# Kernel optimization log

Measured on AMD Instinct MI355X. Metric: run time of the kernel, lower is better.

Reference implementation:

```python
import jax, jax.numpy as jnp
import numpy as np

B, T, S, H, M, V, L = 16, 128, 256, 512, 512, 32000, 2


def setup_inputs() -> dict:
    key = jax.random.key(0)
    ks = jax.random.split(key, 16)
    s = 0.05
    embed = jax.random.normal(ks[3], (V, H), jnp.float32) * 0.02
    embed = embed.at[0].set(0.0)  # padding_idx=0 row is zero in nn.Embedding
    return {
        'tgt': jax.random.randint(ks[0], (B, T), 0, V),
        'hidden': jax.random.normal(ks[1], (L, B, M), jnp.float32) * 0.1,
        'enc_outs': jax.random.normal(ks[2], (B, S, M), jnp.float32) * 0.1,
        'embed': embed,
        'W_ih0': jax.random.normal(ks[4], (3 * M, H), jnp.float32) * s,
        'W_hh0': jax.random.normal(ks[5], (3 * M, M), jnp.float32) * s,
        'b_ih0': jax.random.normal(ks[6], (3 * M,), jnp.float32) * s,
        'b_hh0': jax.random.normal(ks[7], (3 * M,), jnp.float32) * s,
        'W_ih1': jax.random.normal(ks[8], (3 * M, M), jnp.float32) * s,
        'W_hh1': jax.random.normal(ks[9], (3 * M, M), jnp.float32) * s,
        'b_ih1': jax.random.normal(ks[10], (3 * M,), jnp.float32) * s,
        'b_hh1': jax.random.normal(ks[11], (3 * M,), jnp.float32) * s,
        'W_out': jax.random.normal(ks[12], (V, M), jnp.float32) * s,
        'b_out': jax.random.normal(ks[13], (V,), jnp.float32) * s,
    }


def _gru_layer(x, h0, W_ih, W_hh, b_ih, b_hh):
    """PyTorch-convention GRU layer. x: [B,T,in], h0: [B,M] -> (ys [B,T,M], hT [B,M])."""
    # precompute input-side gates for all timesteps: [B,T,3M]
    xg = jnp.einsum('bti,gi->btg', x, W_ih) + b_ih

    def step(h, xg_t):
        gh = h @ W_hh.T + b_hh
        i_r, i_z, i_n = jnp.split(xg_t, 3, axis=-1)
        h_r, h_z, h_n = jnp.split(gh, 3, axis=-1)
        r = jax.nn.sigmoid(i_r + h_r)
        z = jax.nn.sigmoid(i_z + h_z)
        n = jnp.tanh(i_n + r * h_n)
        h_new = (1.0 - z) * n + z * h
        return h_new, h_new

    hT, ys = jax.lax.scan(step, h0, jnp.swapaxes(xg, 0, 1))  # scan over time
    return jnp.swapaxes(ys, 0, 1), hT


def reference(tgt, hidden, enc_outs, embed, W_ih0, W_hh0, b_ih0, b_hh0,
              W_ih1, W_hh1, b_ih1, b_hh1, W_out, b_out):
    x = embed[tgt]  # [B,T,H]
    out0, h0f = _gru_layer(x, hidden[0], W_ih0, W_hh0, b_ih0, b_hh0)
    outputs, h1f = _gru_layer(out0, hidden[1], W_ih1, W_hh1, b_ih1, b_hh1)  # [B,T,M]
    hn = jnp.stack([h0f, h1f])  # [L,B,M]
    cn = jnp.zeros_like(hn)
    # dot-product attention, batched over all timesteps (fuses the per-ts Python loop)
    scores = jnp.einsum('btm,bsm->bts', outputs, enc_outs)
    weights = jax.nn.softmax(scores, axis=-1)
    contexts = jnp.einsum('bts,bsm->btm', weights, enc_outs)
    attn_outs = outputs + contexts
    logits = jnp.einsum('btm,vm->btv', attn_outs, W_out) + b_out  # dropout p=0 -> identity
    return logits, (hn, cn)
```

## Files before the change

kernel.cpp:

```cpp
#include <hip/hip_runtime.h>
#include <hip/hip_bf16.h>
#include <math.h>

#define B_ 16
#define T_ 128
#define S_ 256
#define H_ 512
#define M_ 512
#define V_ 32000

typedef __attribute__((ext_vector_type(8))) short short8v;
typedef __attribute__((ext_vector_type(4))) float float4v;

__global__ __launch_bounds__(128) void k_gather(const int* __restrict__ tgt,
    const float* __restrict__ embed, float* __restrict__ x)
{
  const int row = blockIdx.x;
  const int v = tgt[row];
  const float4* src = (const float4*)(embed + (size_t)v * H_);
  float4* dst = (float4*)(x + (size_t)row * H_);
  dst[threadIdx.x] = src[threadIdx.x];
}

__global__ __launch_bounds__(256) void k_gemm_nt_bias(const float* __restrict__ A,
    const float* __restrict__ Bm, const float* __restrict__ bias,
    float* __restrict__ C, int N)
{
  __shared__ float As[64][33];
  __shared__ float Bs[64][33];
  const int tid = threadIdx.x;
  const int tm = tid >> 4, tn = tid & 15;
  const float* Ab = A  + (size_t)blockIdx.y * 64 * 512;
  const float* Bb = Bm + (size_t)blockIdx.x * 64 * 512;
  float acc00=0.f,acc01=0.f,acc02=0.f,acc03=0.f;
  float acc10=0.f,acc11=0.f,acc12=0.f,acc13=0.f;
  float acc20=0.f,acc21=0.f,acc22=0.f,acc23=0.f;
  float acc30=0.f,acc31=0.f,acc32=0.f,acc33=0.f;
  for (int k0 = 0; k0 < 512; k0 += 32) {
#pragma unroll
    for (int i = 0; i < 8; ++i) {
      int v = tid + i * 256;
      int row = v >> 5, col = v & 31;
      As[row][col] = Ab[(size_t)row * 512 + k0 + col];
      Bs[row][col] = Bb[(size_t)row * 512 + k0 + col];
    }
    __syncthreads();
#pragma unroll
    for (int kk = 0; kk < 32; ++kk) {
      float a0 = As[tm*4+0][kk], a1 = As[tm*4+1][kk];
      float a2 = As[tm*4+2][kk], a3 = As[tm*4+3][kk];
      float b0 = Bs[tn*4+0][kk], b1 = Bs[tn*4+1][kk];
      float b2 = Bs[tn*4+2][kk], b3 = Bs[tn*4+3][kk];
      acc00 += a0*b0; acc01 += a0*b1; acc02 += a0*b2; acc03 += a0*b3;
      acc10 += a1*b0; acc11 += a1*b1; acc12 += a1*b2; acc13 += a1*b3;
      acc20 += a2*b0; acc21 += a2*b1; acc22 += a2*b2; acc23 += a2*b3;
      acc30 += a3*b0; acc31 += a3*b1; acc32 += a3*b2; acc33 += a3*b3;
    }
    __syncthreads();
  }
  const int mbase = blockIdx.y*64 + tm*4;
  const int nbase = blockIdx.x*64 + tn*4;
  float bj0 = bias[nbase+0], bj1 = bias[nbase+1], bj2 = bias[nbase+2], bj3 = bias[nbase+3];
  float* Cr0 = C + (size_t)(mbase+0)*N + nbase;
  float* Cr1 = C + (size_t)(mbase+1)*N + nbase;
  float* Cr2 = C + (size_t)(mbase+2)*N + nbase;
  float* Cr3 = C + (size_t)(mbase+3)*N + nbase;
  Cr0[0]=acc00+bj0; Cr0[1]=acc01+bj1; Cr0[2]=acc02+bj2; Cr0[3]=acc03+bj3;
  Cr1[0]=acc10+bj0; Cr1[1]=acc11+bj1; Cr1[2]=acc12+bj2; Cr1[3]=acc13+bj3;
  Cr2[0]=acc20+bj0; Cr2[1]=acc21+bj1; Cr2[2]=acc22+bj2; Cr2[3]=acc23+bj3;
  Cr3[0]=acc30+bj0; Cr3[1]=acc31+bj1; Cr3[2]=acc32+bj2; Cr3[3]=acc33+bj3;
}

__device__ inline void bulk8_to_lds(const float* rowbase, int sc, float* dstrow)
{
  const float* p = rowbase + sc * 4;
  float4 a, b, c, d, e, f, g, h;
  asm volatile(
    "global_load_dwordx4 %0, %[p], off sc0 sc1\n\t"
    "global_load_dwordx4 %1, %[p], off offset:256 sc0 sc1\n\t"
    "global_load_dwordx4 %2, %[p], off offset:512 sc0 sc1\n\t"
    "global_load_dwordx4 %3, %[p], off offset:768 sc0 sc1\n\t"
    "global_load_dwordx4 %4, %[p], off offset:1024 sc0 sc1\n\t"
    "global_load_dwordx4 %5, %[p], off offset:1280 sc0 sc1\n\t"
    "global_load_dwordx4 %6, %[p], off offset:1536 sc0 sc1\n\t"
    "global_load_dwordx4 %7, %[p], off offset:1792 sc0 sc1\n\t"
    "s_waitcnt vmcnt(0)"
    : "=&v"(a), "=&v"(b), "=&v"(c), "=&v"(d),
      "=&v"(e), "=&v"(f), "=&v"(g), "=&v"(h)
    : [p]"v"(p)
    : "memory");
  *(float4*)&dstrow[(0*16 + sc) * 4] = a;
  *(float4*)&dstrow[(1*16 + sc) * 4] = b;
  *(float4*)&dstrow[(2*16 + sc) * 4] = c;
  *(float4*)&dstrow[(3*16 + sc) * 4] = d;
  *(float4*)&dstrow[(4*16 + sc) * 4] = e;
  *(float4*)&dstrow[(5*16 + sc) * 4] = f;
  *(float4*)&dstrow[(6*16 + sc) * 4] = g;
  *(float4*)&dstrow[(7*16 + sc) * 4] = h;
}

__global__ __launch_bounds__(256) void k_gru2(
    const float* __restrict__ xg0,
    const float* __restrict__ Whh0, const float* __restrict__ bhh0,
    const float* __restrict__ Wih1, const float* __restrict__ bih1,
    const float* __restrict__ Whh1, const float* __restrict__ bhh1,
    const float* __restrict__ hidden,
    float* __restrict__ out0, float* __restrict__ y1, float* __restrict__ hn,
    unsigned int* __restrict__ fA, unsigned int* __restrict__ fB)
{
  __shared__ float Wl[24][520];
  __shared__ float hx[2][16 * 520];
  __shared__ float ps[24][16][17];
  const int bid = blockIdx.x;
  const int lt = threadIdx.x;

  if (bid >= 192) {
    __shared__ int done;
    if (lt == 0) done = 0;
    __syncthreads();
    const unsigned int* flag = &fB[(T_ - 1) * 128 + (bid - 192)];
    float a0 = 1.0f + lt, a1 = 2.0f + lt, a2 = 3.0f, a3 = 4.0f;
    const float mb = 1.0001f, cb = 0.9999f;
    for (;;) {
#pragma unroll 16
      for (int i = 0; i < 512; ++i) {
        a0 = __builtin_fmaf(a0, mb, cb); a1 = __builtin_fmaf(a1, mb, cb);
        a2 = __builtin_fmaf(a2, mb, cb); a3 = __builtin_fmaf(a3, mb, cb);
      }
      if (lt == 0 &&
          __hip_atomic_load(flag, __ATOMIC_RELAXED, __HIP_MEMORY_SCOPE_AGENT) != 0u)
        done = 1;
      __syncthreads();
      if (done) break;
    }
    asm volatile("" :: "v"(a0), "v"(a1), "v"(a2), "v"(a3));
    return;
  }

  const bool isB = bid >= 64;
  const int wg = isB ? bid - 64 : bid;
  const int dbase = isB ? wg * 4 : wg * 8;

  for (int r = 0; r < 24; ++r) {
    const float* src;
    if (!isB) src = Whh0 + (size_t)((r >> 3) * 512 + dbase + (r & 7)) * 512;
    else if (r < 12) src = Whh1 + (size_t)((r >> 2) * 512 + dbase + (r & 3)) * 512;
    else { int rr = r - 12; src = Wih1 + (size_t)((rr >> 2) * 512 + dbase + (rr & 3)) * 512; }
    Wl[r][lt] = src[lt];
    Wl[r][lt + 256] = src[lt + 256];
  }

  const int kq = lt & 15;
  const int bq = (lt >> 4) & 3;
  const int rgrp = lt >> 6;
  const int sb = lt >> 4;
  const int sc = lt & 15;
  float* ybuf = isB ? y1 : out0;
  const float* h0g = hidden + (isB ? 8192 : 0);

  const int rb = isB ? (lt >> 2) : (lt >> 3);
  const int rdl = isB ? (lt & 3) : (lt & 7);
  const int rdg = dbase + rdl;
  const int nred = isB ? 64 : 128;
  float bhr = 0.f, bhz = 0.f, bhn = 0.f, bir = 0.f, biz = 0.f, bin_ = 0.f;
  if (lt < nred) {
    const float* bhh = isB ? bhh1 : bhh0;
    bhr = bhh[rdg]; bhz = bhh[512 + rdg]; bhn = bhh[1024 + rdg];
    if (isB) { bir = bih1[rdg]; biz = bih1[512 + rdg]; bin_ = bih1[1024 + rdg]; }
  }

  for (int t = 0; t < T_; ++t) {
    if (!isB) {
      if (t > 0 && lt < 64) {
        unsigned v;
        do {
          v = __hip_atomic_load(&fA[(t - 1) * 64 + lt], __ATOMIC_RELAXED, __HIP_MEMORY_SCOPE_AGENT);
          if (__all(v != 0u)) break;
          __builtin_amdgcn_s_sleep(1);
        } while (true);
      }
    } else {
      if (lt < 64) {
        unsigned v;
        do {
          v = __hip_atomic_load(&fA[t * 64 + lt], __ATOMIC_RELAXED, __HIP_MEMORY_SCOPE_AGENT);
          if (__all(v != 0u)) break;
          __builtin_amdgcn_s_sleep(1);
        } while (true);
      } else if (t > 0 && lt < 192) {
        unsigned v;
        do {
          v = __hip_atomic_load(&fB[(t - 1) * 128 + (lt - 64)], __ATOMIC_RELAXED, __HIP_MEMORY_SCOPE_AGENT);
          if (__all(v != 0u)) break;
          __builtin_amdgcn_s_sleep(1);
        } while (true);
      }
    }
    __syncthreads();

    if (t == 0) {
#pragma unroll
      for (int j = 0; j < 8; ++j)
        *(float4*)&hx[0][sb * 520 + (j * 16 + sc) * 4] =
            *(const float4*)(h0g + sb * 512 + (j * 16 + sc) * 4);
    } else {
      bulk8_to_lds(ybuf + (size_t)(sb * T_ + t - 1) * 512, sc, &hx[0][sb * 520]);
    }
    if (isB)
      bulk8_to_lds(out0 + (size_t)(sb * T_ + t) * 512, sc, &hx[1][sb * 520]);
    __syncthreads();

    const float* inb = (isB && rgrp >= 2) ? &hx[1][0] : &hx[0][0];
    float acc[6][4];
#pragma unroll
    for (int jr = 0; jr < 6; ++jr)
#pragma unroll
      for (int jb = 0; jb < 4; ++jb) acc[jr][jb] = 0.f;
#pragma unroll
    for (int i = 0; i < 8; ++i) {
      const int kb = kq * 4 + i * 64;
      float4 hv0 = *(const float4*)(inb + (bq * 4 + 0) * 520 + kb);
      float4 hv1 = *(const float4*)(inb + (bq * 4 + 1) * 520 + kb);
      float4 hv2 = *(const float4*)(inb + (bq * 4 + 2) * 520 + kb);
      float4 hv3 = *(const float4*)(inb + (bq * 4 + 3) * 520 + kb);
#pragma unroll
      for (int jr = 0; jr < 6; ++jr) {
        float4 wv = *(const float4*)(&Wl[rgrp * 6 + jr][kb]);
        acc[jr][0] += wv.x*hv0.x + wv.y*hv0.y + wv.z*hv0.z + wv.w*hv0.w;
        acc[jr][1] += wv.x*hv1.x + wv.y*hv1.y + wv.z*hv1.z + wv.w*hv1.w;
        acc[jr][2] += wv.x*hv2.x + wv.y*hv2.y + wv.z*hv2.z + wv.w*hv2.w;
        acc[jr][3] += wv.x*hv3.x + wv.y*hv3.y + wv.z*hv3.z + wv.w*hv3.w;
      }
    }
#pragma unroll
    for (int jr = 0; jr < 6; ++jr)
#pragma unroll
      for (int jb = 0; jb < 4; ++jb)
        ps[rgrp * 6 + jr][bq * 4 + jb][kq] = acc[jr][jb];
    __syncthreads();

    if (lt < nred) {
      float ghr, ghz, ghn, ixr, ixz, ixn;
      if (!isB) {
        float s0 = 0.f, s1 = 0.f, s2 = 0.f;
#pragma unroll
        for (int q = 0; q < 16; ++q) {
          s0 += ps[rdl][rb][q];
          s1 += ps[8 + rdl][rb][q];
          s2 += ps[16 + rdl][rb][q];
        }
        ghr = s0 + bhr; ghz = s1 + bhz; ghn = s2 + bhn;
        const float* xrow = xg0 + (size_t)(rb * T_ + t) * 1536;
        ixr = xrow[rdg]; ixz = xrow[512 + rdg]; ixn = xrow[1024 + rdg];
      } else {
        float s0=0.f,s1=0.f,s2=0.f,s3=0.f,s4=0.f,s5=0.f;
#pragma unroll
        for (int q = 0; q < 16; ++q) {
          s0 += ps[rdl][rb][q];       s1 += ps[4 + rdl][rb][q];  s2 += ps[8 + rdl][rb][q];
          s3 += ps[12 + rdl][rb][q];  s4 += ps[16 + rdl][rb][q]; s5 += ps[20 + rdl][rb][q];
        }
        ghr = s0 + bhr; ghz = s1 + bhz; ghn = s2 + bhn;
        ixr = s3 + bir; ixz = s4 + biz; ixn = s5 + bin_;
      }
      float rr = 1.f / (1.f + expf(-(ixr + ghr)));
      float zz = 1.f / (1.f + expf(-(ixz + ghz)));
      float nn = tanhf(ixn + rr * ghn);
      float hp = hx[0][rb * 520 + rdg];
      float hnew = (1.f - zz) * nn + zz * hp;
      __hip_atomic_store(&ybuf[(size_t)(rb * T_ + t) * 512 + rdg], hnew,
                         __ATOMIC_RELAXED, __HIP_MEMORY_SCOPE_AGENT);
      if (t == T_ - 1) hn[(isB ? 8192 : 0) + rb * 512 + rdg] = hnew;
    }
    __syncthreads();
    if (lt == 0) {
      if (isB)
        __hip_atomic_store(&fB[t * 128 + wg], 1u, __ATOMIC_RELAXED, __HIP_MEMORY_SCOPE_AGENT);
      else
        __hip_atomic_store(&fA[t * 64 + wg], 1u, __ATOMIC_RELAXED, __HIP_MEMORY_SCOPE_AGENT);
    }
  }
}

__global__ __launch_bounds__(256) void k_attn(const float* __restrict__ y,
    const float* __restrict__ enc, float* __restrict__ aout)
{
  __shared__ float orow[512];
  __shared__ float wbuf[256];
  __shared__ float red[8];
  const int row = blockIdx.x;
  const int b = row >> 7;
  const int lt = threadIdx.x;
  orow[lt]       = y[(size_t)row*512 + lt];
  orow[lt + 256] = y[(size_t)row*512 + lt + 256];
  __syncthreads();
  const float* er = enc + (size_t)(b*S_ + lt) * 512;
  float acc = 0.f;
  for (int k = 0; k < 512; k += 4) {
    float4 e = *(const float4*)(er + k);
    acc += orow[k]*e.x + orow[k+1]*e.y + orow[k+2]*e.z + orow[k+3]*e.w;
  }
  float m = acc;
#pragma unroll
  for (int off = 32; off > 0; off >>= 1) m = fmaxf(m, __shfl_down(m, off));
  if ((lt & 63) == 0) red[lt >> 6] = m;
  __syncthreads();
  float mx = fmaxf(fmaxf(red[0], red[1]), fmaxf(red[2], red[3]));
  float e = expf(acc - mx);
  wbuf[lt] = e;
  float s = e;
#pragma unroll
  for (int off = 32; off > 0; off >>= 1) s += __shfl_down(s, off);
  if ((lt & 63) == 0) red[4 + (lt >> 6)] = s;
  __syncthreads();
  const float inv = 1.f / (red[4] + red[5] + red[6] + red[7]);
  const int kk = lt * 2;
  float c0 = 0.f, c1 = 0.f;
  for (int s2 = 0; s2 < S_; ++s2) {
    float ws = wbuf[s2];
    float2 ev = *(const float2*)(enc + (size_t)(b*S_ + s2)*512 + kk);
    c0 += ws * ev.x; c1 += ws * ev.y;
  }
  aout[(size_t)row*512 + kk]     = orow[kk]     + c0 * inv;
  aout[(size_t)row*512 + kk + 1] = orow[kk + 1] + c1 * inv;
}

__global__ __launch_bounds__(256) void k_logits(const float* __restrict__ A,
    const float* __restrict__ Bm, const float* __restrict__ bias,
    float* __restrict__ C)
{
  __shared__ unsigned short Bs[128 * 512];
  __shared__ unsigned short As[128 * 64];
  const int tid = threadIdx.x;
  const int nbase = blockIdx.x * 128;
  const int wv = tid >> 6;
  const int l  = tid & 63;
  const int wr = wv >> 1, wc = wv & 1;
  const int r = l & 15, q = l >> 4;

  for (int i = 0; i < 32; ++i) {
    const int gid = tid + i * 256;
    const int row = gid >> 6, cg = gid & 63;
    const float* Bg = Bm + (size_t)(nbase + row) * 512 + cg * 8;
    float4 g0 = *(const float4*)(Bg);
    float4 g1 = *(const float4*)(Bg + 4);
    union { short8v v; __hip_bfloat162 h2[4]; } pb;
    pb.h2[0] = __float22bfloat162_rn({g0.x, g0.y});
    pb.h2[1] = __float22bfloat162_rn({g0.z, g0.w});
    pb.h2[2] = __float22bfloat162_rn({g1.x, g1.y});
    pb.h2[3] = __float22bfloat162_rn({g1.z, g1.w});
    const int byte = (row * 1024 + cg * 16) ^ ((row & 7) << 4);
    *(short8v*)&Bs[byte >> 1] = pb.v;
  }
  __syncthreads();

  for (int m = 0; m < 16; ++m) {
    const int mbase = m * 128;
    float4v acc[4][4];
#pragma unroll
    for (int mi = 0; mi < 4; ++mi)
#pragma unroll
      for (int ni = 0; ni < 4; ++ni)
        acc[mi][ni] = (float4v){0.f, 0.f, 0.f, 0.f};

    for (int kc = 0; kc < 8; ++kc) {
#pragma unroll
      for (int i = 0; i < 4; ++i) {
        const int gid = tid + i * 256;
        const int row = gid >> 3, cg = gid & 7;
        const float* Ag = A + (size_t)(mbase + row) * 512 + kc * 64 + cg * 8;
        float4 f0 = *(const float4*)(Ag);
        float4 f1 = *(const float4*)(Ag + 4);
        union { short8v v; __hip_bfloat162 h2[4]; } pa;
        pa.h2[0] = __float22bfloat162_rn({f0.x, f0.y});
        pa.h2[1] = __float22bfloat162_rn({f0.z, f0.w});
        pa.h2[2] = __float22bfloat162_rn({f1.x, f1.y});
        pa.h2[3] = __float22bfloat162_rn({f1.z, f1.w});
        const int byte = (row * 128 + cg * 16) ^ ((row & 7) << 4);
        *(short8v*)&As[byte >> 1] = pa.v;
      }
      __syncthreads();

#pragma unroll
      for (int k0s = 0; k0s < 2; ++k0s) {
        short8v af[4], bf[4];
#pragma unroll
        for (int mi = 0; mi < 4; ++mi) {
          const int row = wr * 64 + mi * 16 + r;
          const int byte = (row * 128 + k0s * 64 + q * 16) ^ ((row & 7) << 4);
          af[mi] = *(short8v*)&As[byte >> 1];
        }
#pragma unroll
        for (int ni = 0; ni < 4; ++ni) {
          const int row = wc * 64 + ni * 16 + r;
          const int byte = (row * 1024 + kc * 128 + k0s * 64 + q * 16) ^ ((row & 7) << 4);
          bf[ni] = *(short8v*)&Bs[byte >> 1];
        }
#pragma unroll
        for (int mi = 0; mi < 4; ++mi)
#pragma unroll
          for (int ni = 0; ni < 4; ++ni)
            acc[mi][ni] = __builtin_amdgcn_mfma_f32_16x16x32_bf16(af[mi], bf[ni], acc[mi][ni], 0, 0, 0);
      }
      __syncthreads();
    }

    const int mg = mbase + wr * 64;
    const int ng = nbase + wc * 64;
#pragma unroll
    for (int ni = 0; ni < 4; ++ni) {
      const int col = ng + ni * 16 + r;
      const float bj = bias[col];
#pragma unroll
      for (int mi = 0; mi < 4; ++mi) {
        const int rowb = mg + mi * 16 + q * 4;
        float4v v = acc[mi][ni];
        C[(size_t)(rowb + 0) * V_ + col] = v[0] + bj;
        C[(size_t)(rowb + 1) * V_ + col] = v[1] + bj;
        C[(size_t)(rowb + 2) * V_ + col] = v[2] + bj;
        C[(size_t)(rowb + 3) * V_ + col] = v[3] + bj;
      }
    }
  }
}

extern "C" void kernel_launch(void* const* d_in, const int* in_sizes, int n_in,
                              void* d_out, int out_size, void* d_ws, size_t ws_size,
                              hipStream_t stream)
{
  const int*   tgt    = (const int*)  d_in[0];
  const float* hidden = (const float*)d_in[1];
  const float* enc    = (const float*)d_in[2];
  const float* embed  = (const float*)d_in[3];
  const float* W_ih0  = (const float*)d_in[4];
  const float* W_hh0  = (const float*)d_in[5];
  const float* b_ih0  = (const float*)d_in[6];
  const float* b_hh0  = (const float*)d_in[7];
  const float* W_ih1  = (const float*)d_in[8];
  const float* W_hh1  = (const float*)d_in[9];
  const float* b_ih1  = (const float*)d_in[10];
  const float* b_hh1  = (const float*)d_in[11];
  const float* W_out  = (const float*)d_in[12];
  const float* b_out  = (const float*)d_in[13];
  float* out = (float*)d_out;

  float* ws   = (float*)d_ws;
  float* xbuf = ws;
  float* xg   = ws + 1048576;
  float* out0 = xg + 3145728;
  float* y1   = out0 + 1048576;
  unsigned int* fA = (unsigned int*)(y1 + 1048576);
  unsigned int* fB = fA + T_ * 64;

  const size_t logitsN = (size_t)(B_*T_) * V_;
  float* hn = out + logitsN;
  float* cn = hn + 16384;

  hipMemsetAsync(fA, 0, (size_t)(T_ * 64 + T_ * 128) * sizeof(unsigned int), stream);
  hipMemsetAsync(cn, 0, (size_t)16384 * sizeof(float), stream);

  k_gather<<<dim3(B_*T_), dim3(128), 0, stream>>>(tgt, embed, xbuf);
  k_gemm_nt_bias<<<dim3(1536/64, (B_*T_)/64), dim3(256), 0, stream>>>(xbuf, W_ih0, b_ih0, xg, 1536);
  k_gru2<<<dim3(256), dim3(256), 0, stream>>>(xg, W_hh0, b_hh0, W_ih1, b_ih1,
                                              W_hh1, b_hh1, hidden, out0, y1, hn, fA, fB);
  k_attn<<<dim3(B_*T_), dim3(256), 0, stream>>>(y1, enc, xbuf);
  k_logits<<<dim3(V_/128), dim3(256), 0, stream>>>(xbuf, W_out, b_out, out);
}
```

Before: 1.403 ms.

## Replace GRU flag barriers with sentinel-filled data polling; fuse gather into bf16 MFMA GEMM

The per-step flag arrays and their spin waits are replaced by pre-filling out0/y1 with a NaN sentinel, so consumers poll the data itself until no sentinel remains. This removes one round of flag store/load latency per timestep in the serial recurrence. Separately, the embedding gather is fused into the input-projection GEMM, which now converts to bf16 and uses MFMA instead of scalar fp32. The cost is an extra fill kernel and reduced precision for the input gates, and correctness relies on the sentinel never occurring as a real value and on the 128-byte loads not tearing.

```diff
diff --git a/kernel.cpp b/kernel.cpp
--- a/kernel.cpp
+++ b/kernel.cpp
@@ -8,73 +8,108 @@
 #define H_ 512
 #define M_ 512
 #define V_ 32000
+#define SENT 0x7FC0DEADu
 
 typedef __attribute__((ext_vector_type(8))) short short8v;
 typedef __attribute__((ext_vector_type(4))) float float4v;
 
-__global__ __launch_bounds__(128) void k_gather(const int* __restrict__ tgt,
-    const float* __restrict__ embed, float* __restrict__ x)
-{
-  const int row = blockIdx.x;
-  const int v = tgt[row];
-  const float4* src = (const float4*)(embed + (size_t)v * H_);
-  float4* dst = (float4*)(x + (size_t)row * H_);
-  dst[threadIdx.x] = src[threadIdx.x];
-}
-
-__global__ __launch_bounds__(256) void k_gemm_nt_bias(const float* __restrict__ A,
-    const float* __restrict__ Bm, const float* __restrict__ bias,
-    float* __restrict__ C, int N)
-{
-  __shared__ float As[64][33];
-  __shared__ float Bs[64][33];
+__global__ __launch_bounds__(512) void k_fill(unsigned int* __restrict__ p, int n)
+{
+  const int i = blockIdx.x * 512 + threadIdx.x;
+  if (i < n) p[i] = SENT;
+}
+
+__global__ __launch_bounds__(256) void k_xg_bf16(const int* __restrict__ tgt,
+    const float* __restrict__ embed, const float* __restrict__ Bm,
+    const float* __restrict__ bias, float* __restrict__ C)
+{
+  __shared__ unsigned short As[128 * 40];
+  __shared__ unsigned short Bs[128 * 40];
   const int tid = threadIdx.x;
-  const int tm = tid >> 4, tn = tid & 15;
-  const float* Ab = A  + (size_t)blockIdx.y * 64 * 512;
-  const float* Bb = Bm + (size_t)blockIdx.x * 64 * 512;
-  float acc00=0.f,acc01=0.f,acc02=0.f,acc03=0.f;
-  float acc10=0.f,acc11=0.f,acc12=0.f,acc13=0.f;
-  float acc20=0.f,acc21=0.f,acc22=0.f,acc23=0.f;
-  float acc30=0.f,acc31=0.f,acc32=0.f,acc33=0.f;
+  const int nbase = blockIdx.x * 128;
+  const int mbase = blockIdx.y * 128;
+  const int wv = tid >> 6;
+  const int l  = tid & 63;
+  const int wr = wv >> 1, wc = wv & 1;
+  const int r = l & 15, q = l >> 4;
+
+  const int row0 = tid >> 2, row1 = (tid + 256) >> 2;
+  const int v0 = tgt[mbase + row0];
+  const int v1 = tgt[mbase + row1];
+
+  float4v acc[4][4];
+#pragma unroll
+  for (int mi = 0; mi < 4; ++mi)
+#pragma unroll
+    for (int ni = 0; ni < 4; ++ni)
+      acc[mi][ni] = (float4v){0.f, 0.f, 0.f, 0.f};
+
   for (int k0 = 0; k0 < 512; k0 += 32) {
-#pragma unroll
-    for (int i = 0; i < 8; ++i) {
-      int v = tid + i * 256;
-      int row = v >> 5, col = v & 31;
-      As[row][col] = Ab[(size_t)row * 512 + k0 + col];
-      Bs[row][col] = Bb[(size_t)row * 512 + k0 + col];
-    }
-    __syncthreads();
-#pragma unroll
-    for (int kk = 0; kk < 32; ++kk) {
-      float a0 = As[tm*4+0][kk], a1 = As[tm*4+1][kk];
-      float a2 = As[tm*4+2][kk], a3 = As[tm*4+3][kk];
-      float b0 = Bs[tn*4+0][kk], b1 = Bs[tn*4+1][kk];
-      float b2 = Bs[tn*4+2][kk], b3 = Bs[tn*4+3][kk];
-      acc00 += a0*b0; acc01 += a0*b1; acc02 += a0*b2; acc03 += a0*b3;
-      acc10 += a1*b0; acc11 += a1*b1; acc12 += a1*b2; acc13 += a1*b3;
-      acc20 += a2*b0; acc21 += a2*b1; acc22 += a2*b2; acc23 += a2*b3;
-      acc30 += a3*b0; acc31 += a3*b1; acc32 += a3*b2; acc33 += a3*b3;
-    }
-    __syncthreads();
-  }
-  const int mbase = blockIdx.y*64 + tm*4;
-  const int nbase = blockIdx.x*64 + tn*4;
-  float bj0 = bias[nbase+0], bj1 = bias[nbase+1], bj2 = bias[nbase+2], bj3 = bias[nbase+3];
-  float* Cr0 = C + (size_t)(mbase+0)*N + nbase;
-  float* Cr1 = C + (size_t)(mbase+1)*N + nbase;
-  float* Cr2 = C + (size_t)(mbase+2)*N + nbase;
-  float* Cr3 = C + (size_t)(mbase+3)*N + nbase;
-  Cr0[0]=acc00+bj0; Cr0[1]=acc01+bj1; Cr0[2]=acc02+bj2; Cr0[3]=acc03+bj3;
-  Cr1[0]=acc10+bj0; Cr1[1]=acc11+bj1; Cr1[2]=acc12+bj2; Cr1[3]=acc13+bj3;
-  Cr2[0]=acc20+bj0; Cr2[1]=acc21+bj1; Cr2[2]=acc22+bj2; Cr2[3]=acc23+bj3;
-  Cr3[0]=acc30+bj0; Cr3[1]=acc31+bj1; Cr3[2]=acc32+bj2; Cr3[3]=acc33+bj3;
-}
-
-__device__ inline void bulk8_to_lds(const float* rowbase, int sc, float* dstrow)
-{
+    __syncthreads();
+#pragma unroll
+    for (int h = 0; h < 2; ++h) {
+      const int c = tid + h * 256;
+      const int row = h ? row1 : row0;
+      const int av  = h ? v1 : v0;
+      const int cb = c & 3;
+      const float* Ag = embed + (size_t)av * 512 + k0 + cb * 8;
+      float4 f0 = *(const float4*)(Ag);
+      float4 f1 = *(const float4*)(Ag + 4);
+      union { short8v v; __hip_bfloat162 h2[4]; } pa;
+      pa.h2[0] = __float22bfloat162_rn({f0.x, f0.y});
+      pa.h2[1] = __float22bfloat162_rn({f0.z, f0.w});
+      pa.h2[2] = __float22bfloat162_rn({f1.x, f1.y});
+      pa.h2[3] = __float22bfloat162_rn({f1.z, f1.w});
+      *(short8v*)&As[row * 40 + cb * 8] = pa.v;
+      const float* Bg = Bm + (size_t)(nbase + row) * 512 + k0 + cb * 8;
+      float4 g0 = *(const float4*)(Bg);
+      float4 g1 = *(const float4*)(Bg + 4);
+      union { short8v v; __hip_bfloat162 h2[4]; } pb;
+      pb.h2[0] = __float22bfloat162_rn({g0.x, g0.y});
+      pb.h2[1] = __float22bfloat162_rn({g0.z, g0.w});
+      pb.h2[2] = __float22bfloat162_rn({g1.x, g1.y});
+      pb.h2[3] = __float22bfloat162_rn({g1.z, g1.w});
+      *(short8v*)&Bs[row * 40 + cb * 8] = pb.v;
+    }
+    __syncthreads();
+
+    short8v af[4], bf[4];
+#pragma unroll
+    for (int mi = 0; mi < 4; ++mi)
+      af[mi] = *(short8v*)&As[(wr * 64 + mi * 16 + r) * 40 + q * 8];
+#pragma unroll
+    for (int ni = 0; ni < 4; ++ni)
+      bf[ni] = *(short8v*)&Bs[(wc * 64 + ni * 16 + r) * 40 + q * 8];
+#pragma unroll
+    for (int mi = 0; mi < 4; ++mi)
+#pragma unroll
+      for (int ni = 0; ni < 4; ++ni)
+        acc[mi][ni] = __builtin_amdgcn_mfma_f32_16x16x32_bf16(af[mi], bf[ni], acc[mi][ni], 0, 0, 0);
+  }
+
+  const int mg = mbase + wr * 64;
+  const int ng = nbase + wc * 64;
+#pragma unroll
+  for (int ni = 0; ni < 4; ++ni) {
+    const int col = ng + ni * 16 + r;
+    const float bj = bias[col];
+#pragma unroll
+    for (int mi = 0; mi < 4; ++mi) {
+      const int rowb = mg + mi * 16 + q * 4;
+      float4v v = acc[mi][ni];
+      C[(size_t)(rowb + 0) * 1536 + col] = v[0] + bj;
+      C[(size_t)(rowb + 1) * 1536 + col] = v[1] + bj;
+      C[(size_t)(rowb + 2) * 1536 + col] = v[2] + bj;
+      C[(size_t)(rowb + 3) * 1536 + col] = v[3] + bj;
+    }
+  }
+}
+
+struct F4x8 { float4 a, b, c, d, e, f, g, h; };
+__device__ inline F4x8 bulk8_ld(const float* rowbase, int sc)
+{
+  F4x8 r;
   const float* p = rowbase + sc * 4;
-  float4 a, b, c, d, e, f, g, h;
   asm volatile(
     "global_load_dwordx4 %0, %[p], off sc0 sc1\n\t"
     "global_load_dwordx4 %1, %[p], off offset:256 sc0 sc1\n\t"
@@ -85,18 +120,38 @@
     "global_load_dwordx4 %6, %[p], off offset:1536 sc0 sc1\n\t"
     "global_load_dwordx4 %7, %[p], off offset:1792 sc0 sc1\n\t"
     "s_waitcnt vmcnt(0)"
-    : "=&v"(a), "=&v"(b), "=&v"(c), "=&v"(d),
-      "=&v"(e), "=&v"(f), "=&v"(g), "=&v"(h)
+    : "=&v"(r.a), "=&v"(r.b), "=&v"(r.c), "=&v"(r.d),
+      "=&v"(r.e), "=&v"(r.f), "=&v"(r.g), "=&v"(r.h)
     : [p]"v"(p)
     : "memory");
-  *(float4*)&dstrow[(0*16 + sc) * 4] = a;
-  *(float4*)&dstrow[(1*16 + sc) * 4] = b;
-  *(float4*)&dstrow[(2*16 + sc) * 4] = c;
-  *(float4*)&dstrow[(3*16 + sc) * 4] = d;
-  *(float4*)&dstrow[(4*16 + sc) * 4] = e;
-  *(float4*)&dstrow[(5*16 + sc) * 4] = f;
-  *(float4*)&dstrow[(6*16 + sc) * 4] = g;
-  *(float4*)&dstrow[(7*16 + sc) * 4] = h;
+  return r;
+}
+
+__device__ inline bool anysent(const F4x8& r)
+{
+  auto c1 = [](float4 v) {
+    return (__float_as_uint(v.x) == SENT) | (__float_as_uint(v.y) == SENT) |
+           (__float_as_uint(v.z) == SENT) | (__float_as_uint(v.w) == SENT);
+  };
+  return c1(r.a) | c1(r.b) | c1(r.c) | c1(r.d) |
+         c1(r.e) | c1(r.f) | c1(r.g) | c1(r.h);
+}
+
+__device__ inline void stage_sent(const float* rowbase, int sc, float* dstrow)
+{
+  F4x8 r = bulk8_ld(rowbase, sc);
+  while (anysent(r)) {
+    __builtin_amdgcn_s_sleep(1);
+    r = bulk8_ld(rowbase, sc);
+  }
+  *(float4*)&dstrow[(0*16 + sc) * 4] = r.a;
+  *(float4*)&dstrow[(1*16 + sc) * 4] = r.b;
+  *(float4*)&dstrow[(2*16 + sc) * 4] = r.c;
+  *(float4*)&dstrow[(3*16 + sc) * 4] = r.d;
+  *(float4*)&dstrow[(4*16 + sc) * 4] = r.e;
+  *(float4*)&dstrow[(5*16 + sc) * 4] = r.f;
+  *(float4*)&dstrow[(6*16 + sc) * 4] = r.g;
+  *(float4*)&dstrow[(7*16 + sc) * 4] = r.h;
 }
 
 __global__ __launch_bounds__(256) void k_gru2(
@@ -105,8 +160,7 @@
     const float* __restrict__ Wih1, const float* __restrict__ bih1,
     const float* __restrict__ Whh1, const float* __restrict__ bhh1,
     const float* __restrict__ hidden,
-    float* __restrict__ out0, float* __restrict__ y1, float* __restrict__ hn,
-    unsigned int* __restrict__ fA, unsigned int* __restrict__ fB)
+    float* __restrict__ out0, float* __restrict__ y1, float* __restrict__ hn)
 {
   __shared__ float Wl[24][520];
   __shared__ float hx[2][16 * 520];
@@ -118,7 +172,7 @@
     __shared__ int done;
     if (lt == 0) done = 0;
     __syncthreads();
-    const unsigned int* flag = &fB[(T_ - 1) * 128 + (bid - 192)];
+    const float* flag = y1 + (size_t)(15 * T_ + 127) * 512 + 511;
     float a0 = 1.0f + lt, a1 = 2.0f + lt, a2 = 3.0f, a3 = 4.0f;
     const float mb = 1.0001f, cb = 0.9999f;
     for (;;) {
@@ -128,7 +182,8 @@
         a2 = __builtin_fmaf(a2, mb, cb); a3 = __builtin_fmaf(a3, mb, cb);
       }
       if (lt == 0 &&
-          __hip_atomic_load(flag, __ATOMIC_RELAXED, __HIP_MEMORY_SCOPE_AGENT) != 0u)
+          __float_as_uint(__hip_atomic_load(flag, __ATOMIC_RELAXED,
+                                            __HIP_MEMORY_SCOPE_AGENT)) != SENT)
         done = 1;
       __syncthreads();
       if (done) break;
@@ -168,46 +223,19 @@
     bhr = bhh[rdg]; bhz = bhh[512 + rdg]; bhn = bhh[1024 + rdg];
     if (isB) { bir = bih1[rdg]; biz = bih1[512 + rdg]; bin_ = bih1[1024 + rdg]; }
   }
+  __syncthreads();
 
   for (int t = 0; t < T_; ++t) {
-    if (!isB) {
-      if (t > 0 && lt < 64) {
-        unsigned v;
-        do {
-          v = __hip_atomic_load(&fA[(t - 1) * 64 + lt], __ATOMIC_RELAXED, __HIP_MEMORY_SCOPE_AGENT);
-          if (__all(v != 0u)) break;
-          __builtin_amdgcn_s_sleep(1);
-        } while (true);
-      }
-    } else {
-      if (lt < 64) {
-        unsigned v;
-        do {
-          v = __hip_atomic_load(&fA[t * 64 + lt], __ATOMIC_RELAXED, __HIP_MEMORY_SCOPE_AGENT);
-          if (__all(v != 0u)) break;
-          __builtin_amdgcn_s_sleep(1);
-        } while (true);
-      } else if (t > 0 && lt < 192) {
-        unsigned v;
-        do {
-          v = __hip_atomic_load(&fB[(t - 1) * 128 + (lt - 64)], __ATOMIC_RELAXED, __HIP_MEMORY_SCOPE_AGENT);
-          if (__all(v != 0u)) break;
-          __builtin_amdgcn_s_sleep(1);
-        } while (true);
-      }
-    }
-    __syncthreads();
-
     if (t == 0) {
 #pragma unroll
       for (int j = 0; j < 8; ++j)
         *(float4*)&hx[0][sb * 520 + (j * 16 + sc) * 4] =
             *(const float4*)(h0g + sb * 512 + (j * 16 + sc) * 4);
     } else {
-      bulk8_to_lds(ybuf + (size_t)(sb * T_ + t - 1) * 512, sc, &hx[0][sb * 520]);
+      stage_sent(ybuf + (size_t)(sb * T_ + t - 1) * 512, sc, &hx[0][sb * 520]);
     }
     if (isB)
-      bulk8_to_lds(out0 + (size_t)(sb * T_ + t) * 512, sc, &hx[1][sb * 520]);
+      stage_sent(out0 + (size_t)(sb * T_ + t) * 512, sc, &hx[1][sb * 520]);
     __syncthreads();
 
     const float* inb = (isB && rgrp >= 2) ? &hx[1][0] : &hx[0][0];
@@ -272,12 +300,6 @@
       if (t == T_ - 1) hn[(isB ? 8192 : 0) + rb * 512 + rdg] = hnew;
     }
     __syncthreads();
-    if (lt == 0) {
-      if (isB)
-        __hip_atomic_store(&fB[t * 128 + wg], 1u, __ATOMIC_RELAXED, __HIP_MEMORY_SCOPE_AGENT);
-      else
-        __hip_atomic_store(&fA[t * 64 + wg], 1u, __ATOMIC_RELAXED, __HIP_MEMORY_SCOPE_AGENT);
-    }
   }
 }
 
@@ -448,20 +470,17 @@
   float* xg   = ws + 1048576;
   float* out0 = xg + 3145728;
   float* y1   = out0 + 1048576;
-  unsigned int* fA = (unsigned int*)(y1 + 1048576);
-  unsigned int* fB = fA + T_ * 64;
 
   const size_t logitsN = (size_t)(B_*T_) * V_;
   float* hn = out + logitsN;
   float* cn = hn + 16384;
 
-  hipMemsetAsync(fA, 0, (size_t)(T_ * 64 + T_ * 128) * sizeof(unsigned int), stream);
   hipMemsetAsync(cn, 0, (size_t)16384 * sizeof(float), stream);
 
-  k_gather<<<dim3(B_*T_), dim3(128), 0, stream>>>(tgt, embed, xbuf);
-  k_gemm_nt_bias<<<dim3(1536/64, (B_*T_)/64), dim3(256), 0, stream>>>(xbuf, W_ih0, b_ih0, xg, 1536);
+  k_fill<<<dim3(4096), dim3(512), 0, stream>>>((unsigned int*)out0, 2097152);
+  k_xg_bf16<<<dim3(1536/128, 2048/128), dim3(256), 0, stream>>>(tgt, embed, W_ih0, b_ih0, xg);
   k_gru2<<<dim3(256), dim3(256), 0, stream>>>(xg, W_hh0, b_hh0, W_ih1, b_ih1,
-                                              W_hh1, b_hh1, hidden, out0, y1, hn, fA, fB);
+                                              W_hh1, b_hh1, hidden, out0, y1, hn);
   k_attn<<<dim3(B_*T_), dim3(256), 0, stream>>>(y1, enc, xbuf);
   k_logits<<<dim3(V_/128), dim3(256), 0, stream>>>(xbuf, W_out, b_out, out);
 }
```

After: 1.326 ms. -5.5%, faster.
